# Kernel optimization log

Measured on AMD Instinct MI355X. Metric: run time of the kernel, lower is better.

Reference implementation:

```python
import jax, jax.numpy as jnp
import numpy as np
import math

B, S, D = 16, 512, 1024
H, L = 16, 4
DH = D // H
EPS = 1e-5


def _layernorm(x, w, b):
    mu = jnp.mean(x, axis=-1, keepdims=True)
    var = jnp.mean(jnp.square(x - mu), axis=-1, keepdims=True)
    return (x - mu) / jnp.sqrt(var + EPS) * w + b


def _pos_encoding(s, d):
    pos = jnp.arange(s, dtype=jnp.float32)[:, None]                      # [s,1]
    div = jnp.exp(jnp.arange(0, d, 2, dtype=jnp.float32) * (-math.log(10000.0) / d))
    ang = pos * div[None, :]                                             # [s,d/2]
    return jnp.stack([jnp.sin(ang), jnp.cos(ang)], axis=-1).reshape(s, d)  # interleave sin/cos


def _attention_layer(x, Wq, bq, Wv, bv, Wo, bo, gamma, ln_w, ln_b, mask):
    bs, s, d = x.shape
    # q_linear == k_linear (kq_same=True)
    q = (x @ Wq.T + bq).reshape(bs, s, H, DH).transpose(0, 2, 1, 3)      # [b,h,s,dh]
    k = q
    v = (x @ Wv.T + bv).reshape(bs, s, H, DH).transpose(0, 2, 1, 3)

    scores = jnp.einsum('bhqd,bhkd->bhqk', q, k) / math.sqrt(DH)         # [b,h,s,s]

    # distance-decay modulation (dist_scores is detached in the original)
    p = jax.nn.softmax(jnp.where(mask, scores, -1e32), axis=-1)
    distcum = jnp.cumsum(p, axis=-1)
    disttot = jnp.sum(p, axis=-1, keepdims=True)
    idx = jnp.arange(s, dtype=jnp.float32)
    pos_eff = jnp.abs(idx[None, :] - idx[:, None])[None, None, :, :]     # |i-j|
    dist = jnp.sqrt(jnp.maximum((disttot - distcum) * pos_eff, 0.0))
    dist = jax.lax.stop_gradient(dist)

    g = -jnp.abs(gamma)[None, :, None, None]                             # [1,h,1,1]
    total_effect = jnp.clip(jnp.exp(dist * g), 1e-5, 1e5)
    scores = scores * total_effect

    scores = jnp.where(mask, scores, -1e32)
    attn = jax.nn.softmax(scores, axis=-1)
    attn = jnp.where(mask, attn, 0.0)

    # maxout=True (peek_cur=False): clamp(1/max, max=5)
    scale = jnp.minimum(1.0 / jnp.max(attn, axis=-1, keepdims=True), 5.0)
    attn = attn * scale

    out = jnp.einsum('bhqk,bhkd->bhqd', attn, v)                         # [b,h,s,dh]
    out = out.transpose(0, 2, 1, 3).reshape(bs, s, d)
    out = out @ Wo.T + bo

    # eval mode: dropout = identity; residual + layernorm
    return _layernorm(x + out, ln_w, ln_b), attn


def reference(x, lens, Wq, bq, Wv, bv, Wo, bo, gammas, ln_w, ln_b, fln_w, fln_b):
    del lens  # only used in training-mode random masking
    s = x.shape[1]
    q = x + _pos_encoding(s, D)[None, :, :]
    mask = jnp.tril(jnp.ones((s, s), dtype=bool), -1)[None, None, :, :]  # peek_cur=False
    scores = None
    for l in range(L):
        q, scores = _attention_layer(q, Wq[l], bq[l], Wv[l], bv[l], Wo[l], bo[l],
                                     gammas[l], ln_w[l], ln_b[l], mask)
    return _layernorm(q, fln_w, fln_b), scores


def setup_inputs() -> dict:
    key = jax.random.key(0)
    ks = jax.random.split(key, 8)
    wscale = 1.0 / math.sqrt(D)
    return {
        'x': jax.random.normal(ks[0], (B, S, D), dtype=jnp.float32),
        'lens': jax.random.randint(ks[1], (B,), 1, S),
        'Wq': jax.random.normal(ks[2], (L, D, D), dtype=jnp.float32) * wscale,
        'bq': jnp.zeros((L, D), dtype=jnp.float32),
        'Wv': jax.random.normal(ks[3], (L, D, D), dtype=jnp.float32) * wscale,
        'bv': jnp.zeros((L, D), dtype=jnp.float32),
        'Wo': jax.random.normal(ks[4], (L, D, D), dtype=jnp.float32) * wscale,
        'bo': jnp.zeros((L, D), dtype=jnp.float32),
        'gammas': jax.random.uniform(ks[5], (L, H), dtype=jnp.float32, minval=-1.7, maxval=1.7),
        'ln_w': jnp.ones((L, D), dtype=jnp.float32),
        'ln_b': jnp.zeros((L, D), dtype=jnp.float32),
        'fln_w': jnp.ones((D,), dtype=jnp.float32),
        'fln_b': jnp.zeros((D,), dtype=jnp.float32),
    }
```

## Files before the change

### kernel.cpp

```cpp
#include <hip/hip_runtime.h>
#include <hip/hip_bf16.h>

#define BB 16
#define SS 512
#define DD 1024
#define HH 16
#define LL 4
#define DHH 64
#define GK 1024

typedef __attribute__((ext_vector_type(8))) short short8;
typedef __attribute__((ext_vector_type(4))) float f32x4;

__device__ __forceinline__ unsigned short f2bf(float f) {
  union { float f; unsigned int u; } v; v.f = f;
  unsigned int r = v.u + 0x7FFFu + ((v.u >> 16) & 1u);
  return (unsigned short)(r >> 16);
}

__device__ __forceinline__ float wave_max(float v) {
#pragma unroll
  for (int off = 32; off > 0; off >>= 1) v = fmaxf(v, __shfl_xor(v, off));
  return v;
}
__device__ __forceinline__ float wave_sum(float v) {
#pragma unroll
  for (int off = 32; off > 0; off >>= 1) v += __shfl_xor(v, off);
  return v;
}
__device__ __forceinline__ float half_max(float v) {
#pragma unroll
  for (int off = 16; off > 0; off >>= 1) v = fmaxf(v, __shfl_xor(v, off));
  return v;
}
__device__ __forceinline__ float half_sum(float v) {
#pragma unroll
  for (int off = 16; off > 0; off >>= 1) v += __shfl_xor(v, off);
  return v;
}

__device__ __forceinline__ void gl16(const void* g, void* l) {
  __builtin_amdgcn_global_load_lds(
      (const __attribute__((address_space(1))) unsigned int*)(uintptr_t)g,
      (__attribute__((address_space(3))) unsigned int*)(unsigned int)(uintptr_t)l,
      16, 0, 0);
}

__global__ __launch_bounds__(256) void k_w2bf_all(
    const float* __restrict__ wq, const float* __restrict__ wv,
    const float* __restrict__ wo, unsigned short* __restrict__ oqv,
    unsigned short* __restrict__ oo) {
  size_t i4 = ((size_t)blockIdx.x * 256 + threadIdx.x) * 4;
  const size_t QV = (size_t)2 * LL * DD * DD;
  const float* src;
  unsigned short* dst;
  if (i4 < QV) {
    size_t l = i4 >> 21;
    size_t r = i4 & ((1u << 21) - 1);
    src = (r < (1u << 20)) ? wq + (l << 20) + r
                           : wv + (l << 20) + (r - (1u << 20));
    dst = oqv + i4;
  } else {
    size_t j = i4 - QV;
    src = wo + j;
    dst = oo + j;
  }
  float4 v = *(const float4*)src;
  uint2 pk;
  pk.x = (unsigned)f2bf(v.x) | ((unsigned)f2bf(v.y) << 16);
  pk.y = (unsigned)f2bf(v.z) | ((unsigned)f2bf(v.w) << 16);
  *(uint2*)dst = pk;
}

__global__ __launch_bounds__(256) void k_add_pe(const float* __restrict__ x,
                                                float* __restrict__ out,
                                                unsigned short* __restrict__ outb) {
  size_t i4 = ((size_t)blockIdx.x * 256 + threadIdx.x) * 4;
  int d0 = (int)(i4 & (DD - 1));
  int s = (int)((i4 >> 10) & (SS - 1));
  float4 xv = *(const float4*)(x + i4);
  int ip0 = d0 >> 1;
  float f0 = __expf((float)ip0 * -0.017988946039016f);
  float f1 = __expf((float)(ip0 + 1) * -0.017988946039016f);
  float s0v, c0v, s1v, c1v;
  __sincosf((float)s * f0, &s0v, &c0v);
  __sincosf((float)s * f1, &s1v, &c1v);
  float4 o;
  o.x = xv.x + s0v; o.y = xv.y + c0v; o.z = xv.z + s1v; o.w = xv.w + c1v;
  *(float4*)(out + i4) = o;
  uint2 pk;
  pk.x = (unsigned)f2bf(o.x) | ((unsigned)f2bf(o.y) << 16);
  pk.y = (unsigned)f2bf(o.z) | ((unsigned)f2bf(o.w) << 16);
  *(uint2*)(outb + i4) = pk;
}

template <int MODE>
__global__ __launch_bounds__(256) void k_gemm(
    const unsigned short* __restrict__ A, const unsigned short* __restrict__ W,
    const float* __restrict__ bias, const float* __restrict__ bias2,
    void* __restrict__ out, void* __restrict__ out2) {
  __shared__ unsigned short As[2][128 * 32];
  __shared__ unsigned short Bs[2][128 * 32];
  const int tid = threadIdx.x;
  const int lane = tid & 63;
  const int w = tid >> 6;
  const int wr = w >> 1, wc = w & 1;
  const int fr = lane & 15, fq = lane >> 4;

  int bid = blockIdx.x;
  const int cpx = gridDim.x >> 3;
  bid = (bid & 7) * cpx + (bid >> 3);
  const int bm = (bid & 63) * 128;
  const int bn = (bid >> 6) * 128;

  f32x4 acc[4][4] = {};

  const unsigned short* ga = A + (size_t)(bm + w * 16 + (lane >> 2)) * GK + (lane & 3) * 8;
  const unsigned short* gb = W + (size_t)(bn + w * 16 + (lane >> 2)) * GK + (lane & 3) * 8;

  auto STAGE = [&](int buf, int k0) {
    unsigned short* la = As[buf] + w * 512;
    unsigned short* lb = Bs[buf] + w * 512;
    gl16(ga + k0, la);
    gl16(ga + 64 * GK + k0, la + 2048);
    gl16(gb + k0, lb);
    gl16(gb + 64 * GK + k0, lb + 2048);
  };

  STAGE(0, 0);
  __syncthreads();
  int cur = 0;
  for (int k0 = 0; k0 < GK; k0 += 32) {
    if (k0 + 32 < GK) STAGE(cur ^ 1, k0 + 32);
    short8 af[4], bf[4];
#pragma unroll
    for (int m = 0; m < 4; ++m)
      af[m] = *(const short8*)(As[cur] + (wr * 64 + m * 16 + fr) * 32 + fq * 8);
#pragma unroll
    for (int n = 0; n < 4; ++n)
      bf[n] = *(const short8*)(Bs[cur] + (wc * 64 + n * 16 + fr) * 32 + fq * 8);
#pragma unroll
    for (int m = 0; m < 4; ++m)
#pragma unroll
      for (int n = 0; n < 4; ++n)
        acc[m][n] = __builtin_amdgcn_mfma_f32_16x16x32_bf16(af[m], bf[n], acc[m][n], 0, 0, 0);
    __syncthreads();
    cur ^= 1;
  }

#pragma unroll
  for (int m = 0; m < 4; ++m) {
    const int row0 = bm + wr * 64 + m * 16 + fq * 4;
#pragma unroll
    for (int n = 0; n < 4; ++n) {
      const int col = bn + wc * 64 + n * 16 + fr;
      if constexpr (MODE == 0) {
        const float bsv = bias[col];
        unsigned short* o = (unsigned short*)out;
#pragma unroll
        for (int r = 0; r < 4; ++r)
          o[(size_t)(row0 + r) * DD + col] = f2bf(acc[m][n][r] + bsv);
      } else if constexpr (MODE == 2) {
        const float bsv = bias[col];
        float* o = (float*)out;
#pragma unroll
        for (int r = 0; r < 4; ++r)
          o[(size_t)(row0 + r) * DD + col] = acc[m][n][r] + bsv;
      } else {
        if (col < DD) {
          const float bsv = bias[col];
          unsigned short* o = (unsigned short*)out;
#pragma unroll
          for (int r = 0; r < 4; ++r)
            o[(size_t)(row0 + r) * DD + col] = f2bf(acc[m][n][r] + bsv);
        } else {
          const int c2 = col - DD;
          const float bsv = bias2[c2];
          unsigned short* o = (unsigned short*)out2;
          const int bi = row0 >> 9, si = row0 & (SS - 1);
          uint2 pk;
          pk.x = (unsigned)f2bf(acc[m][n][0] + bsv) | ((unsigned)f2bf(acc[m][n][1] + bsv) << 16);
          pk.y = (unsigned)f2bf(acc[m][n][2] + bsv) | ((unsigned)f2bf(acc[m][n][3] + bsv) << 16);
          *(uint2*)(o + ((size_t)bi * DD + c2) * SS + si) = pk;
        }
      }
    }
  }
}

__global__ __launch_bounds__(512) void k_attn_big(
    const unsigned short* __restrict__ Q, const unsigned short* __restrict__ Vt,
    const float* __restrict__ gam, unsigned short* __restrict__ AO,
    float* __restrict__ scores_out) {
  __shared__ float sc_s[32][516];
  __shared__ unsigned short KV[64][72];

  const int tid = threadIdx.x;
  const int lane = tid & 63;
  const int w = tid >> 6;
  const int wr = w & 1;
  const int wc = w >> 1;
  const int fr = lane & 15, fq = lane >> 4;

  const int itile = 8 + (blockIdx.x & 7);
  const int bh = blockIdx.x >> 3;
  const int b = bh >> 4;
  const int h = bh & 15;
  const int i0 = itile * 32;
  const int njt = (itile + 2) >> 1;
  const int jcap = njt * 64;

  const unsigned short* Qb = Q + (size_t)b * SS * DD + h * DHH;
  const unsigned short* Vtb = Vt + ((size_t)b * DD + h * DHH) * SS;
  const float gneg = -fabsf(gam[h]);

  const int srow = tid >> 3;
  const int sdb = (tid & 7) * 8;

  const unsigned short* qrow = Qb + (size_t)(i0 + wr * 16 + fr) * DD;
  short8 a0 = *(const short8*)(qrow + fq * 8);
  short8 a1 = *(const short8*)(qrow + 32 + fq * 8);

  short8 kreg = *(const short8*)(Qb + (size_t)srow * DD + sdb);
  for (int jt = 0; jt < njt; ++jt) {
    *(short8*)&KV[srow][sdb] = kreg;
    const unsigned short* nsrc = (jt + 1 < njt)
        ? Qb + (size_t)((jt + 1) * 64 + srow) * DD + sdb
        : Vtb + (size_t)srow * SS + sdb;
    kreg = *(const short8*)nsrc;
    __syncthreads();

    short8 b0 = *(const short8*)&KV[wc * 16 + fr][fq * 8];
    short8 b1 = *(const short8*)&KV[wc * 16 + fr][32 + fq * 8];
    f32x4 s0 = {};
    s0 = __builtin_amdgcn_mfma_f32_16x16x32_bf16(a0, b0, s0, 0, 0, 0);
    s0 = __builtin_amdgcn_mfma_f32_16x16x32_bf16(a1, b1, s0, 0, 0, 0);

    const int j = jt * 64 + wc * 16 + fr;
#pragma unroll
    for (int r = 0; r < 4; ++r) {
      const int row = wr * 16 + fq * 4 + r;
      sc_s[row][j] = (j < i0 + row) ? s0[r] * 0.125f : -1e30f;
    }
    __syncthreads();
  }
  *(short8*)&KV[srow][sdb] = kreg;

  const int jb = lane << 3;
#pragma unroll 2
  for (int q = 0; q < 4; ++q) {
    const int r_i = w * 4 + q;
    const int gi = i0 + r_i;
    const float* rowp = &sc_s[r_i][0];
    float4 v0 = *(const float4*)(rowp + jb);
    float4 v1 = *(const float4*)(rowp + jb + 4);
    float sc[8] = {v0.x, v0.y, v0.z, v0.w, v1.x, v1.y, v1.z, v1.w};
#pragma unroll
    for (int c = 0; c < 8; ++c)
      if (jb + c >= jcap) sc[c] = -1e30f;

    float p[8];
    float lsum = 0.0f;
#pragma unroll
    for (int c = 0; c < 8; ++c) {
      p[c] = __expf(sc[c]);
      lsum += p[c];
    }

    float xs = lsum;
#pragma unroll
    for (int off = 1; off < 64; off <<= 1) {
      float y = __shfl_up(xs, off);
      if (lane >= off) xs += y;
    }
    const float tot = __shfl(xs, 63);
    const float inv = 1.0f / tot;
    float run = xs - lsum;

    float s2[8];
#pragma unroll
    for (int c = 0; c < 8; ++c) {
      run += p[c];
      float cum = run * inv;
      float dist = sqrtf(fmaxf((1.0f - cum) * (float)(gi - (jb + c)), 0.0f));
      float te = __expf(gneg * dist);
      te = fminf(fmaxf(te, 1e-5f), 1e5f);
      s2[c] = sc[c] * te;
    }

    float m2 = s2[0];
#pragma unroll
    for (int c = 1; c < 8; ++c) m2 = fmaxf(m2, s2[c]);
    m2 = wave_max(m2);
    float e[8];
    float lsum2 = 0.0f;
#pragma unroll
    for (int c = 0; c < 8; ++c) {
      e[c] = __expf(s2[c] - m2);
      lsum2 += e[c];
    }
    float tot2 = wave_sum(lsum2);
    float mult = fminf(tot2, 5.0f) / tot2;

    float av[8];
#pragma unroll
    for (int c = 0; c < 8; ++c) {
      av[c] = (gi == 0) ? 0.0f : e[c] * mult;
    }

    if (scores_out) {
      float* so = scores_out + ((size_t)(b * HH + h) * SS + gi) * SS + jb;
      *(float4*)(so) = make_float4(av[0], av[1], av[2], av[3]);
      *(float4*)(so + 4) = make_float4(av[4], av[5], av[6], av[7]);
    }

    short8 pk;
#pragma unroll
    for (int c = 0; c < 8; ++c) pk[c] = (short)f2bf(av[c]);
    *(short8*)((unsigned short*)&sc_s[r_i][0] + jb) = pk;
  }
  __syncthreads();

  short8 vreg;
  if (njt > 1) vreg = *(const short8*)(Vtb + (size_t)srow * SS + 64 + sdb);
  f32x4 o0 = {};
  for (int jt = 0; jt < njt; ++jt) {
    const unsigned short* arow = (const unsigned short*)&sc_s[wr * 16 + fr][0];
    short8 pa0 = *(const short8*)(arow + jt * 64 + fq * 8);
    short8 pa1 = *(const short8*)(arow + jt * 64 + 32 + fq * 8);
    short8 c0 = *(const short8*)&KV[wc * 16 + fr][fq * 8];
    short8 c1 = *(const short8*)&KV[wc * 16 + fr][32 + fq * 8];
    o0 = __builtin_amdgcn_mfma_f32_16x16x32_bf16(pa0, c0, o0, 0, 0, 0);
    o0 = __builtin_amdgcn_mfma_f32_16x16x32_bf16(pa1, c1, o0, 0, 0, 0);
    __syncthreads();
    if (jt + 1 < njt) {
      *(short8*)&KV[srow][sdb] = vreg;
      if (jt + 2 < njt) vreg = *(const short8*)(Vtb + (size_t)srow * SS + (jt + 2) * 64 + sdb);
      __syncthreads();
    }
  }

  {
    const int d = h * DHH + wc * 16 + fr;
#pragma unroll
    for (int r = 0; r < 4; ++r) {
      const int row = i0 + wr * 16 + fq * 4 + r;
      AO[((size_t)b * SS + row) * DD + d] = f2bf(o0[r]);
    }
  }
}

__global__ __launch_bounds__(512) void k_attn_small(
    const unsigned short* __restrict__ Q, const unsigned short* __restrict__ Vt,
    const float* __restrict__ gam, unsigned short* __restrict__ AO,
    float* __restrict__ scores_out) {
  __shared__ float sc_s[32][260];
  __shared__ unsigned short KV[64][72];

  const int tid = threadIdx.x;
  const int lane = tid & 63;
  const int w = tid >> 6;
  const int wr = w & 1;
  const int wc = w >> 1;
  const int fr = lane & 15, fq = lane >> 4;

  const int itile = blockIdx.x & 7;
  const int bh = blockIdx.x >> 3;
  const int b = bh >> 4;
  const int h = bh & 15;
  const int i0 = itile * 32;
  const int njt = (itile + 2) >> 1;
  const int jcap = njt * 64;

  const unsigned short* Qb = Q + (size_t)b * SS * DD + h * DHH;
  const unsigned short* Vtb = Vt + ((size_t)b * DD + h * DHH) * SS;
  const float gneg = -fabsf(gam[h]);

  const int srow = tid >> 3;
  const int sdb = (tid & 7) * 8;

  const unsigned short* qrow = Qb + (size_t)(i0 + wr * 16 + fr) * DD;
  short8 a0 = *(const short8*)(qrow + fq * 8);
  short8 a1 = *(const short8*)(qrow + 32 + fq * 8);

  short8 kreg = *(const short8*)(Qb + (size_t)srow * DD + sdb);
  for (int jt = 0; jt < njt; ++jt) {
    *(short8*)&KV[srow][sdb] = kreg;
    const unsigned short* nsrc = (jt + 1 < njt)
        ? Qb + (size_t)((jt + 1) * 64 + srow) * DD + sdb
        : Vtb + (size_t)srow * SS + sdb;
    kreg = *(const short8*)nsrc;
    __syncthreads();

    short8 b0 = *(const short8*)&KV[wc * 16 + fr][fq * 8];
    short8 b1 = *(const short8*)&KV[wc * 16 + fr][32 + fq * 8];
    f32x4 s0 = {};
    s0 = __builtin_amdgcn_mfma_f32_16x16x32_bf16(a0, b0, s0, 0, 0, 0);
    s0 = __builtin_amdgcn_mfma_f32_16x16x32_bf16(a1, b1, s0, 0, 0, 0);

    const int j = jt * 64 + wc * 16 + fr;
#pragma unroll
    for (int r = 0; r < 4; ++r) {
      const int row = wr * 16 + fq * 4 + r;
      sc_s[row][j] = (j < i0 + row) ? s0[r] * 0.125f : -1e30f;
    }
    __syncthreads();
  }
  *(short8*)&KV[srow][sdb] = kreg;

  const int half = lane >> 5;
  const int ll = lane & 31;
  const int jb = ll << 3;
  for (int q = 0; q < 2; ++q) {
    const int r_i = w * 4 + q * 2 + half;
    const int gi = i0 + r_i;
    const float* rowp = &sc_s[r_i][0];
    float4 v0 = *(const float4*)(rowp + jb);
    float4 v1 = *(const float4*)(rowp + jb + 4);
    float sc[8] = {v0.x, v0.y, v0.z, v0.w, v1.x, v1.y, v1.z, v1.w};
#pragma unroll
    for (int c = 0; c < 8; ++c)
      if (jb + c >= jcap) sc[c] = -1e30f;

    float p[8];
    float lsum = 0.0f;
#pragma unroll
    for (int c = 0; c < 8; ++c) {
      p[c] = __expf(sc[c]);
      lsum += p[c];
    }

    float xs = lsum;
#pragma unroll
    for (int off = 1; off < 32; off <<= 1) {
      float y = __shfl_up(xs, off, 32);
      if (ll >= off) xs += y;
    }
    const float tot = __shfl(xs, 31, 32);
    const float inv = 1.0f / tot;
    float run = xs - lsum;

    float s2[8];
#pragma unroll
    for (int c = 0; c < 8; ++c) {
      run += p[c];
      float cum = run * inv;
      float dist = sqrtf(fmaxf((1.0f - cum) * (float)(gi - (jb + c)), 0.0f));
      float te = __expf(gneg * dist);
      te = fminf(fmaxf(te, 1e-5f), 1e5f);
      s2[c] = sc[c] * te;
    }

    float m2 = s2[0];
#pragma unroll
    for (int c = 1; c < 8; ++c) m2 = fmaxf(m2, s2[c]);
    m2 = half_max(m2);
    float e[8];
    float lsum2 = 0.0f;
#pragma unroll
    for (int c = 0; c < 8; ++c) {
      e[c] = __expf(s2[c] - m2);
      lsum2 += e[c];
    }
    const float tot2 = half_sum(lsum2);
    const float mult = fminf(tot2, 5.0f) / tot2;

    float av[8];
#pragma unroll
    for (int c = 0; c < 8; ++c) {
      av[c] = (gi == 0) ? 0.0f : e[c] * mult;
    }

    if (scores_out) {
      float* so = scores_out + ((size_t)(b * HH + h) * SS + gi) * SS + jb;
      *(float4*)(so) = make_float4(av[0], av[1], av[2], av[3]);
      *(float4*)(so + 4) = make_float4(av[4], av[5], av[6], av[7]);
      *(float4*)(so + 256) = make_float4(0.f, 0.f, 0.f, 0.f);
      *(float4*)(so + 260) = make_float4(0.f, 0.f, 0.f, 0.f);
    }

    short8 pk;
#pragma unroll
    for (int c = 0; c < 8; ++c) pk[c] = (short)f2bf(av[c]);
    *(short8*)((unsigned short*)&sc_s[r_i][0] + jb) = pk;
  }
  __syncthreads();

  short8 vreg;
  if (njt > 1) vreg = *(const short8*)(Vtb + (size_t)srow * SS + 64 + sdb);
  f32x4 o0 = {};
  for (int jt = 0; jt < njt; ++jt) {
    const unsigned short* arow = (const unsigned short*)&sc_s[wr * 16 + fr][0];
    short8 pa0 = *(const short8*)(arow + jt * 64 + fq * 8);
    short8 pa1 = *(const short8*)(arow + jt * 64 + 32 + fq * 8);
    short8 c0 = *(const short8*)&KV[wc * 16 + fr][fq * 8];
    short8 c1 = *(const short8*)&KV[wc * 16 + fr][32 + fq * 8];
    o0 = __builtin_amdgcn_mfma_f32_16x16x32_bf16(pa0, c0, o0, 0, 0, 0);
    o0 = __builtin_amdgcn_mfma_f32_16x16x32_bf16(pa1, c1, o0, 0, 0, 0);
    __syncthreads();
    if (jt + 1 < njt) {
      *(short8*)&KV[srow][sdb] = vreg;
      if (jt + 2 < njt) vreg = *(const short8*)(Vtb + (size_t)srow * SS + (jt + 2) * 64 + sdb);
      __syncthreads();
    }
  }

  {
    const int d = h * DHH + wc * 16 + fr;
#pragma unroll
    for (int r = 0; r < 4; ++r) {
      const int row = i0 + wr * 16 + fq * 4 + r;
      AO[((size_t)b * SS + row) * DD + d] = f2bf(o0[r]);
    }
  }
}

__global__ __launch_bounds__(256) void k_res_ln(
    const float* __restrict__ x, const float* __restrict__ r,
    const float* __restrict__ w, const float* __restrict__ b,
    float* __restrict__ out, unsigned short* __restrict__ outb) {
  __shared__ float red[4];
  const int row = blockIdx.x;
  const int tid = threadIdx.x;
  const int lane = tid & 63, wv = tid >> 6;
  float4 y = ((const float4*)(x + (size_t)row * DD))[tid];
  if (r) {
    float4 rr = ((const float4*)(r + (size_t)row * DD))[tid];
    y.x += rr.x; y.y += rr.y; y.z += rr.z; y.w += rr.w;
  }
  float s = y.x + y.y + y.z + y.w;
  s = wave_sum(s);
  if (lane == 0) red[wv] = s;
  __syncthreads();
  float mean = (red[0] + red[1] + red[2] + red[3]) * (1.0f / DD);
  __syncthreads();
  float d0 = y.x - mean, d1 = y.y - mean, d2 = y.z - mean, d3 = y.w - mean;
  float s2 = d0 * d0 + d1 * d1 + d2 * d2 + d3 * d3;
  s2 = wave_sum(s2);
  if (lane == 0) red[wv] = s2;
  __syncthreads();
  float var = (red[0] + red[1] + red[2] + red[3]) * (1.0f / DD);
  float rstd = rsqrtf(var + 1e-5f);
  float4 ww = ((const float4*)w)[tid];
  float4 bb = ((const float4*)b)[tid];
  float4 o;
  o.x = d0 * rstd * ww.x + bb.x;
  o.y = d1 * rstd * ww.y + bb.y;
  o.z = d2 * rstd * ww.z + bb.z;
  o.w = d3 * rstd * ww.w + bb.w;
  ((float4*)(out + (size_t)row * DD))[tid] = o;
  if (outb) {
    uint2 pk;
    pk.x = (unsigned)f2bf(o.x) | ((unsigned)f2bf(o.y) << 16);
    pk.y = (unsigned)f2bf(o.z) | ((unsigned)f2bf(o.w) << 16);
    *(uint2*)(outb + (size_t)row * DD + tid * 4) = pk;
  }
}

extern "C" void kernel_launch(void* const* d_in, const int* in_sizes, int n_in,
                              void* d_out, int out_size, void* d_ws, size_t ws_size,
                              hipStream_t stream) {
  (void)in_sizes; (void)n_in; (void)out_size; (void)ws_size;
  const float* x = (const float*)d_in[0];
  const float* Wq = (const float*)d_in[2];
  const float* bq = (const float*)d_in[3];
  const float* Wv = (const float*)d_in[4];
  const float* bv = (const float*)d_in[5];
  const float* Wo = (const float*)d_in[6];
  const float* bo = (const float*)d_in[7];
  const float* gam = (const float*)d_in[8];
  const float* lnw = (const float*)d_in[9];
  const float* lnb = (const float*)d_in[10];
  const float* flnw = (const float*)d_in[11];
  const float* flnb = (const float*)d_in[12];

  float* out0 = (float*)d_out;
  float* scores = out0 + (size_t)BB * SS * DD;
  const size_t BUF = (size_t)BB * SS * DD;
  const size_t WSZ = (size_t)LL * DD * DD;
  const size_t BHSS = (size_t)BB * HH * SS * SS;

  float* P0 = (float*)d_ws;
  float* P1 = P0 + BUF;
  unsigned short* us = (unsigned short*)(P1 + BUF);
  unsigned short* Abf = us;
  unsigned short* Qbf = us + BUF;
  unsigned short* VtB = us + 2 * BUF;
  unsigned short* AObf = us + 3 * BUF;
  unsigned short* Wob = us + 4 * BUF;
  unsigned short* Wqvb = (unsigned short*)scores + (2 * BHSS - 2 * WSZ);

  const int M = BB * SS;

  k_w2bf_all<<<dim3(3 * WSZ / 1024), 256, 0, stream>>>(Wq, Wv, Wo, Wqvb, Wob);
  k_add_pe<<<dim3(BUF / 1024), 256, 0, stream>>>(x, P0, Abf);

  float* Acur = P0;
  float* Pnx = P1;
  for (int l = 0; l < LL; ++l) {
    float* sc_dst = (l == LL - 1) ? scores : nullptr;
    k_gemm<3><<<dim3(1024), 256, 0, stream>>>(Abf, Wqvb + (size_t)l * 2048 * DD,
                                              bq + l * DD, bv + l * DD, Qbf, VtB);
    k_attn_small<<<dim3(BB * HH * 8), 512, 0, stream>>>(Qbf, VtB, gam + l * HH, AObf, sc_dst);
    k_attn_big<<<dim3(BB * HH * 8), 512, 0, stream>>>(Qbf, VtB, gam + l * HH, AObf, sc_dst);
    k_gemm<2><<<dim3(512), 256, 0, stream>>>(AObf, Wob + (size_t)l * DD * DD,
                                             bo + l * DD, nullptr, Pnx, nullptr);
    k_res_ln<<<dim3(M), 256, 0, stream>>>(Acur, Pnx, lnw + l * DD, lnb + l * DD, Pnx, Abf);
    float* t = Acur; Acur = Pnx; Pnx = t;
  }
  k_res_ln<<<dim3(M), 256, 0, stream>>>(Acur, nullptr, flnw, flnb, out0, nullptr);
}
```

Before: 905.6 us.

## Merge small and big attention kernels into one launch with heavy-first tile order

Result: faster. 863.4 us (-4.7%).

```diff
diff --git a/kernel.cpp b/kernel.cpp
--- a/kernel.cpp
+++ b/kernel.cpp
@@ -188,7 +188,7 @@
   }
 }
 
-__global__ __launch_bounds__(512) void k_attn_big(
+__global__ __launch_bounds__(512) void k_attn(
     const unsigned short* __restrict__ Q, const unsigned short* __restrict__ Vt,
     const float* __restrict__ gam, unsigned short* __restrict__ AO,
     float* __restrict__ scores_out) {
@@ -202,8 +202,8 @@
   const int wc = w >> 1;
   const int fr = lane & 15, fq = lane >> 4;
 
-  const int itile = 8 + (blockIdx.x & 7);
-  const int bh = blockIdx.x >> 3;
+  const int itile = 15 - (blockIdx.x >> 8);
+  const int bh = blockIdx.x & 255;
   const int b = bh >> 4;
   const int h = bh & 15;
   const int i0 = itile * 32;
@@ -246,243 +246,153 @@
   }
   *(short8*)&KV[srow][sdb] = kreg;
 
-  const int jb = lane << 3;
+  if (itile >= 8) {
+    const int jb = lane << 3;
 #pragma unroll 2
-  for (int q = 0; q < 4; ++q) {
-    const int r_i = w * 4 + q;
-    const int gi = i0 + r_i;
-    const float* rowp = &sc_s[r_i][0];
-    float4 v0 = *(const float4*)(rowp + jb);
-    float4 v1 = *(const float4*)(rowp + jb + 4);
-    float sc[8] = {v0.x, v0.y, v0.z, v0.w, v1.x, v1.y, v1.z, v1.w};
-#pragma unroll
-    for (int c = 0; c < 8; ++c)
-      if (jb + c >= jcap) sc[c] = -1e30f;
-
-    float p[8];
-    float lsum = 0.0f;
-#pragma unroll
-    for (int c = 0; c < 8; ++c) {
-      p[c] = __expf(sc[c]);
-      lsum += p[c];
+    for (int q = 0; q < 4; ++q) {
+      const int r_i = w * 4 + q;
+      const int gi = i0 + r_i;
+      const float* rowp = &sc_s[r_i][0];
+      float4 v0 = *(const float4*)(rowp + jb);
+      float4 v1 = *(const float4*)(rowp + jb + 4);
+      float sc[8] = {v0.x, v0.y, v0.z, v0.w, v1.x, v1.y, v1.z, v1.w};
+#pragma unroll
+      for (int c = 0; c < 8; ++c)
+        if (jb + c >= jcap) sc[c] = -1e30f;
+
+      float p[8];
+      float lsum = 0.0f;
+#pragma unroll
+      for (int c = 0; c < 8; ++c) {
+        p[c] = __expf(sc[c]);
+        lsum += p[c];
+      }
+
+      float xs = lsum;
+#pragma unroll
+      for (int off = 1; off < 64; off <<= 1) {
+        float y = __shfl_up(xs, off);
+        if (lane >= off) xs += y;
+      }
+      const float tot = __shfl(xs, 63);
+      const float inv = 1.0f / tot;
+      float run = xs - lsum;
+
+      float s2[8];
+#pragma unroll
+      for (int c = 0; c < 8; ++c) {
+        run += p[c];
+        float cum = run * inv;
+        float dist = sqrtf(fmaxf((1.0f - cum) * (float)(gi - (jb + c)), 0.0f));
+        float te = __expf(gneg * dist);
+        te = fminf(fmaxf(te, 1e-5f), 1e5f);
+        s2[c] = sc[c] * te;
+      }
+
+      float m2 = s2[0];
+#pragma unroll
+      for (int c = 1; c < 8; ++c) m2 = fmaxf(m2, s2[c]);
+      m2 = wave_max(m2);
+      float e[8];
+      float lsum2 = 0.0f;
+#pragma unroll
+      for (int c = 0; c < 8; ++c) {
+        e[c] = __expf(s2[c] - m2);
+        lsum2 += e[c];
+      }
+      float tot2 = wave_sum(lsum2);
+      float mult = fminf(tot2, 5.0f) / tot2;
+
+      float av[8];
+#pragma unroll
+      for (int c = 0; c < 8; ++c) av[c] = (gi == 0) ? 0.0f : e[c] * mult;
+
+      if (scores_out) {
+        float* so = scores_out + ((size_t)(b * HH + h) * SS + gi) * SS + jb;
+        *(float4*)(so) = make_float4(av[0], av[1], av[2], av[3]);
+        *(float4*)(so + 4) = make_float4(av[4], av[5], av[6], av[7]);
+      }
+
+      short8 pk;
+#pragma unroll
+      for (int c = 0; c < 8; ++c) pk[c] = (short)f2bf(av[c]);
+      *(short8*)((unsigned short*)&sc_s[r_i][0] + jb) = pk;
     }
-
-    float xs = lsum;
-#pragma unroll
-    for (int off = 1; off < 64; off <<= 1) {
-      float y = __shfl_up(xs, off);
-      if (lane >= off) xs += y;
+  } else {
+    const int half = lane >> 5;
+    const int ll = lane & 31;
+    const int jb = ll << 3;
+    for (int q = 0; q < 2; ++q) {
+      const int r_i = w * 4 + q * 2 + half;
+      const int gi = i0 + r_i;
+      const float* rowp = &sc_s[r_i][0];
+      float4 v0 = *(const float4*)(rowp + jb);
+      float4 v1 = *(const float4*)(rowp + jb + 4);
+      float sc[8] = {v0.x, v0.y, v0.z, v0.w, v1.x, v1.y, v1.z, v1.w};
+#pragma unroll
+      for (int c = 0; c < 8; ++c)
+        if (jb + c >= jcap) sc[c] = -1e30f;
+
+      float p[8];
+      float lsum = 0.0f;
+#pragma unroll
+      for (int c = 0; c < 8; ++c) {
+        p[c] = __expf(sc[c]);
+        lsum += p[c];
+      }
+
+      float xs = lsum;
+#pragma unroll
+      for (int off = 1; off < 32; off <<= 1) {
+        float y = __shfl_up(xs, off, 32);
+        if (ll >= off) xs += y;
+      }
+      const float tot = __shfl(xs, 31, 32);
+      const float inv = 1.0f / tot;
+      float run = xs - lsum;
+
+      float s2[8];
+#pragma unroll
+      for (int c = 0; c < 8; ++c) {
+        run += p[c];
+        float cum = run * inv;
+        float dist = sqrtf(fmaxf((1.0f - cum) * (float)(gi - (jb + c)), 0.0f));
+        float te = __expf(gneg * dist);
+        te = fminf(fmaxf(te, 1e-5f), 1e5f);
+        s2[c] = sc[c] * te;
+      }
+
+      float m2 = s2[0];
+#pragma unroll
+      for (int c = 1; c < 8; ++c) m2 = fmaxf(m2, s2[c]);
+      m2 = half_max(m2);
+      float e[8];
+      float lsum2 = 0.0f;
+#pragma unroll
+      for (int c = 0; c < 8; ++c) {
+        e[c] = __expf(s2[c] - m2);
+        lsum2 += e[c];
+      }
+      const float tot2 = half_sum(lsum2);
+      const float mult = fminf(tot2, 5.0f) / tot2;
+
+      float av[8];
+#pragma unroll
+      for (int c = 0; c < 8; ++c) av[c] = (gi == 0) ? 0.0f : e[c] * mult;
+
+      if (scores_out) {
+        float* so = scores_out + ((size_t)(b * HH + h) * SS + gi) * SS + jb;
+        *(float4*)(so) = make_float4(av[0], av[1], av[2], av[3]);
+        *(float4*)(so + 4) = make_float4(av[4], av[5], av[6], av[7]);
+        *(float4*)(so + 256) = make_float4(0.f, 0.f, 0.f, 0.f);
+        *(float4*)(so + 260) = make_float4(0.f, 0.f, 0.f, 0.f);
+      }
+
+      short8 pk;
+#pragma unroll
+      for (int c = 0; c < 8; ++c) pk[c] = (short)f2bf(av[c]);
+      *(short8*)((unsigned short*)&sc_s[r_i][0] + jb) = pk;
     }
-    const float tot = __shfl(xs, 63);
-    const float inv = 1.0f / tot;
-    float run = xs - lsum;
-
-    float s2[8];
-#pragma unroll
-    for (int c = 0; c < 8; ++c) {
-      run += p[c];
-      float cum = run * inv;
-      float dist = sqrtf(fmaxf((1.0f - cum) * (float)(gi - (jb + c)), 0.0f));
-      float te = __expf(gneg * dist);
-      te = fminf(fmaxf(te, 1e-5f), 1e5f);
-      s2[c] = sc[c] * te;
-    }
-
-    float m2 = s2[0];
-#pragma unroll
-    for (int c = 1; c < 8; ++c) m2 = fmaxf(m2, s2[c]);
-    m2 = wave_max(m2);
-    float e[8];
-    float lsum2 = 0.0f;
-#pragma unroll
-    for (int c = 0; c < 8; ++c) {
-      e[c] = __expf(s2[c] - m2);
-      lsum2 += e[c];
-    }
-    float tot2 = wave_sum(lsum2);
-    float mult = fminf(tot2, 5.0f) / tot2;
-
-    float av[8];
-#pragma unroll
-    for (int c = 0; c < 8; ++c) {
-      av[c] = (gi == 0) ? 0.0f : e[c] * mult;
-    }
-
-    if (scores_out) {
-      float* so = scores_out + ((size_t)(b * HH + h) * SS + gi) * SS + jb;
-      *(float4*)(so) = make_float4(av[0], av[1], av[2], av[3]);
-      *(float4*)(so + 4) = make_float4(av[4], av[5], av[6], av[7]);
-    }
-
-    short8 pk;
-#pragma unroll
-    for (int c = 0; c < 8; ++c) pk[c] = (short)f2bf(av[c]);
-    *(short8*)((unsigned short*)&sc_s[r_i][0] + jb) = pk;
-  }
-  __syncthreads();
-
-  short8 vreg;
-  if (njt > 1) vreg = *(const short8*)(Vtb + (size_t)srow * SS + 64 + sdb);
-  f32x4 o0 = {};
-  for (int jt = 0; jt < njt; ++jt) {
-    const unsigned short* arow = (const unsigned short*)&sc_s[wr * 16 + fr][0];
-    short8 pa0 = *(const short8*)(arow + jt * 64 + fq * 8);
-    short8 pa1 = *(const short8*)(arow + jt * 64 + 32 + fq * 8);
-    short8 c0 = *(const short8*)&KV[wc * 16 + fr][fq * 8];
-    short8 c1 = *(const short8*)&KV[wc * 16 + fr][32 + fq * 8];
-    o0 = __builtin_amdgcn_mfma_f32_16x16x32_bf16(pa0, c0, o0, 0, 0, 0);
-    o0 = __builtin_amdgcn_mfma_f32_16x16x32_bf16(pa1, c1, o0, 0, 0, 0);
-    __syncthreads();
-    if (jt + 1 < njt) {
-      *(short8*)&KV[srow][sdb] = vreg;
-      if (jt + 2 < njt) vreg = *(const short8*)(Vtb + (size_t)srow * SS + (jt + 2) * 64 + sdb);
-      __syncthreads();
-    }
-  }
-
-  {
-    const int d = h * DHH + wc * 16 + fr;
-#pragma unroll
-    for (int r = 0; r < 4; ++r) {
-      const int row = i0 + wr * 16 + fq * 4 + r;
-      AO[((size_t)b * SS + row) * DD + d] = f2bf(o0[r]);
-    }
-  }
-}
-
-__global__ __launch_bounds__(512) void k_attn_small(
-    const unsigned short* __restrict__ Q, const unsigned short* __restrict__ Vt,
-    const float* __restrict__ gam, unsigned short* __restrict__ AO,
-    float* __restrict__ scores_out) {
-  __shared__ float sc_s[32][260];
-  __shared__ unsigned short KV[64][72];
-
-  const int tid = threadIdx.x;
-  const int lane = tid & 63;
-  const int w = tid >> 6;
-  const int wr = w & 1;
-  const int wc = w >> 1;
-  const int fr = lane & 15, fq = lane >> 4;
-
-  const int itile = blockIdx.x & 7;
-  const int bh = blockIdx.x >> 3;
-  const int b = bh >> 4;
-  const int h = bh & 15;
-  const int i0 = itile * 32;
-  const int njt = (itile + 2) >> 1;
-  const int jcap = njt * 64;
-
-  const unsigned short* Qb = Q + (size_t)b * SS * DD + h * DHH;
-  const unsigned short* Vtb = Vt + ((size_t)b * DD + h * DHH) * SS;
-  const float gneg = -fabsf(gam[h]);
-
-  const int srow = tid >> 3;
-  const int sdb = (tid & 7) * 8;
-
-  const unsigned short* qrow = Qb + (size_t)(i0 + wr * 16 + fr) * DD;
-  short8 a0 = *(const short8*)(qrow + fq * 8);
-  short8 a1 = *(const short8*)(qrow + 32 + fq * 8);
-
-  short8 kreg = *(const short8*)(Qb + (size_t)srow * DD + sdb);
-  for (int jt = 0; jt < njt; ++jt) {
-    *(short8*)&KV[srow][sdb] = kreg;
-    const unsigned short* nsrc = (jt + 1 < njt)
-        ? Qb + (size_t)((jt + 1) * 64 + srow) * DD + sdb
-        : Vtb + (size_t)srow * SS + sdb;
-    kreg = *(const short8*)nsrc;
-    __syncthreads();
-
-    short8 b0 = *(const short8*)&KV[wc * 16 + fr][fq * 8];
-    short8 b1 = *(const short8*)&KV[wc * 16 + fr][32 + fq * 8];
-    f32x4 s0 = {};
-    s0 = __builtin_amdgcn_mfma_f32_16x16x32_bf16(a0, b0, s0, 0, 0, 0);
-    s0 = __builtin_amdgcn_mfma_f32_16x16x32_bf16(a1, b1, s0, 0, 0, 0);
-
-    const int j = jt * 64 + wc * 16 + fr;
-#pragma unroll
-    for (int r = 0; r < 4; ++r) {
-      const int row = wr * 16 + fq * 4 + r;
-      sc_s[row][j] = (j < i0 + row) ? s0[r] * 0.125f : -1e30f;
-    }
-    __syncthreads();
-  }
-  *(short8*)&KV[srow][sdb] = kreg;
-
-  const int half = lane >> 5;
-  const int ll = lane & 31;
-  const int jb = ll << 3;
-  for (int q = 0; q < 2; ++q) {
-    const int r_i = w * 4 + q * 2 + half;
-    const int gi = i0 + r_i;
-    const float* rowp = &sc_s[r_i][0];
-    float4 v0 = *(const float4*)(rowp + jb);
-    float4 v1 = *(const float4*)(rowp + jb + 4);
-    float sc[8] = {v0.x, v0.y, v0.z, v0.w, v1.x, v1.y, v1.z, v1.w};
-#pragma unroll
-    for (int c = 0; c < 8; ++c)
-      if (jb + c >= jcap) sc[c] = -1e30f;
-
-    float p[8];
-    float lsum = 0.0f;
-#pragma unroll
-    for (int c = 0; c < 8; ++c) {
-      p[c] = __expf(sc[c]);
-      lsum += p[c];
-    }
-
-    float xs = lsum;
-#pragma unroll
-    for (int off = 1; off < 32; off <<= 1) {
-      float y = __shfl_up(xs, off, 32);
-      if (ll >= off) xs += y;
-    }
-    const float tot = __shfl(xs, 31, 32);
-    const float inv = 1.0f / tot;
-    float run = xs - lsum;
-
-    float s2[8];
-#pragma unroll
-    for (int c = 0; c < 8; ++c) {
-      run += p[c];
-      float cum = run * inv;
-      float dist = sqrtf(fmaxf((1.0f - cum) * (float)(gi - (jb + c)), 0.0f));
-      float te = __expf(gneg * dist);
-      te = fminf(fmaxf(te, 1e-5f), 1e5f);
-      s2[c] = sc[c] * te;
-    }
-
-    float m2 = s2[0];
-#pragma unroll
-    for (int c = 1; c < 8; ++c) m2 = fmaxf(m2, s2[c]);
-    m2 = half_max(m2);
-    float e[8];
-    float lsum2 = 0.0f;
-#pragma unroll
-    for (int c = 0; c < 8; ++c) {
-      e[c] = __expf(s2[c] - m2);
-      lsum2 += e[c];
-    }
-    const float tot2 = half_sum(lsum2);
-    const float mult = fminf(tot2, 5.0f) / tot2;
-
-    float av[8];
-#pragma unroll
-    for (int c = 0; c < 8; ++c) {
-      av[c] = (gi == 0) ? 0.0f : e[c] * mult;
-    }
-
-    if (scores_out) {
-      float* so = scores_out + ((size_t)(b * HH + h) * SS + gi) * SS + jb;
-      *(float4*)(so) = make_float4(av[0], av[1], av[2], av[3]);
-      *(float4*)(so + 4) = make_float4(av[4], av[5], av[6], av[7]);
-      *(float4*)(so + 256) = make_float4(0.f, 0.f, 0.f, 0.f);
-      *(float4*)(so + 260) = make_float4(0.f, 0.f, 0.f, 0.f);
-    }
-
-    short8 pk;
-#pragma unroll
-    for (int c = 0; c < 8; ++c) pk[c] = (short)f2bf(av[c]);
-    *(short8*)((unsigned short*)&sc_s[r_i][0] + jb) = pk;
   }
   __syncthreads();
 
@@ -601,8 +511,7 @@
     float* sc_dst = (l == LL - 1) ? scores : nullptr;
     k_gemm<3><<<dim3(1024), 256, 0, stream>>>(Abf, Wqvb + (size_t)l * 2048 * DD,
                                               bq + l * DD, bv + l * DD, Qbf, VtB);
-    k_attn_small<<<dim3(BB * HH * 8), 512, 0, stream>>>(Qbf, VtB, gam + l * HH, AObf, sc_dst);
-    k_attn_big<<<dim3(BB * HH * 8), 512, 0, stream>>>(Qbf, VtB, gam + l * HH, AObf, sc_dst);
+    k_attn<<<dim3(BB * HH * 16), 512, 0, stream>>>(Qbf, VtB, gam + l * HH, AObf, sc_dst);
     k_gemm<2><<<dim3(512), 256, 0, stream>>>(AObf, Wob + (size_t)l * DD * DD,
                                              bo + l * DD, nullptr, Pnx, nullptr);
     k_res_ln<<<dim3(M), 256, 0, stream>>>(Acur, Pnx, lnw + l * DD, lnb + l * DD, Pnx, Abf);
```
